# Kernel tuning notes

Hardware: AMD Instinct MI355X
Metric: run time of the kernel (lower is better)

## Reference

```python
import jax, jax.numpy as jnp
import numpy as np

B, D_K, D_V = 1024, 64, 64
N_FEAT, RANK, K = 32768, 1, 32

def _normalize(a):
    return a / jnp.linalg.norm(a, axis=-1, keepdims=True)

def setup_inputs() -> dict:
    key = jax.random.key(0)
    k0, k1, k2, k3, k4 = jax.random.split(key, 5)
    x = jax.random.normal(k0, (B, D_K, D_V), dtype=jnp.float32)
    V_enc = _normalize(jax.random.normal(k1, (N_FEAT, RANK, D_K), dtype=jnp.float32))
    W_enc = _normalize(jax.random.normal(k2, (N_FEAT, RANK, D_V), dtype=jnp.float32))
    V_dec = _normalize(jax.random.normal(k3, (N_FEAT, RANK, D_K), dtype=jnp.float32))
    W_dec = _normalize(jax.random.normal(k4, (N_FEAT, RANK, D_V), dtype=jnp.float32))
    b_enc = jnp.zeros((N_FEAT,), dtype=jnp.float32)
    bias = jnp.zeros((D_K, D_V), dtype=jnp.float32)
    return {"x": x, "V_enc": V_enc, "W_enc": W_enc, "b_enc": b_enc,
            "V_dec": V_dec, "W_dec": W_dec, "bias": bias}

def reference(x, V_enc, W_enc, b_enc, V_dec, W_dec, bias):
    b, d_k, d_v = x.shape
    n_feat = V_enc.shape[0]
    x_flat = x.reshape(b, d_k * d_v)
    # encode: einsum('irk,bkv,irv->bi') == x_flat @ (sum_r v_ir (x) w_ir)^T
    M_enc = jnp.einsum('irk,irv->ikv', V_enc, W_enc).reshape(n_feat, d_k * d_v)
    pre = x_flat @ M_enc.T + b_enc                       # [B, n_feat]
    # topk activation with relu on the kept values, zeros elsewhere
    vals, idx = jax.lax.top_k(pre, K)                    # [B, K]
    vals = jnp.maximum(vals, 0.0)
    coeffs = jnp.zeros_like(pre).at[jnp.arange(b)[:, None], idx].set(vals)
    # decode: einsum('bi,irk,irv->bkv')
    M_dec = jnp.einsum('irk,irv->ikv', V_dec, W_dec).reshape(n_feat, d_k * d_v)
    recon_flat = coeffs @ M_dec + bias.reshape(-1)
    recon = recon_flat.reshape(b, d_k, d_v)
    mse = jnp.mean((recon_flat - x_flat) ** 2)
    # fresh steps_since_active buffer (zeros) + dead_threshold=100 -> no dead
    # features, so aux_loss == 0 exactly; total loss == mse.
    return recon, coeffs, mse
```

## Files before the change

### kernel.cpp

```cpp
#include <hip/hip_runtime.h>
#include <hip/hip_bf16.h>
#include <hip/hip_fp8.h>
#include <stdint.h>

#define NFEAT 32768
#define BATCH 1024
#define DK 64
#define DV 64
#define DD 4096
#define KSEL 32
#define CAND_CAP 512
#define CAND_TARGET 128

using bf16 = __bf16;
using f32x4 = __attribute__((ext_vector_type(4))) float;
using f32x16 = __attribute__((ext_vector_type(16))) float;
using i32x4 = __attribute__((ext_vector_type(4))) int;
using i32x8 = __attribute__((ext_vector_type(8))) int;

__device__ __forceinline__ void gload_lds16(const void* g, void* l) {
  __builtin_amdgcn_global_load_lds((const __attribute__((address_space(1))) void*)g,
                                   (__attribute__((address_space(3))) void*)l,
                                   16, 0, 0);
}

__device__ inline unsigned mono16(unsigned u) {
  return (u & 0x8000u) ? ((~u) & 0xFFFFu) : (u | 0x8000u);
}


__global__ void k_convert_x(const float* __restrict__ x, unsigned char* __restrict__ xb) {
  int t = threadIdx.x;
  int rb = blockIdx.x >> 3;
  int kg0 = (blockIdx.x & 7) * 16;
  int row = (t & 127) >> 2;
  int cin = ((t >> 7) << 4) + ((t & 3) << 2);
  const float* xrow = x + ((size_t)rb * 32 + row) * DD;
  for (int kg = kg0; kg < kg0 + 16; ++kg) {
    float4 v = *reinterpret_cast<const float4*>(xrow + kg * 32 + cin);
    union { unsigned char b[4]; unsigned u; } o;
    o.b[0] = __hip_fp8_e4m3(v.x).__x;
    o.b[1] = __hip_fp8_e4m3(v.y).__x;
    o.b[2] = __hip_fp8_e4m3(v.z).__x;
    o.b[3] = __hip_fp8_e4m3(v.w).__x;
    *reinterpret_cast<unsigned*>(xb + (((size_t)rb * 128 + kg) << 10) + t * 4) = o.u;
  }
}

__global__ void k_build_menc(const float* __restrict__ Venc, const float* __restrict__ Wenc,
                             unsigned char* __restrict__ Menc) {
  int t = threadIdx.x;
  int rb = blockIdx.x;
  int row = (t & 127) >> 2;
  int cin = ((t >> 7) << 4) + ((t & 3) << 2);
  size_t rowg = (size_t)rb * 32 + row;
  const float* vrow = Venc + rowg * DK;
  float4 w0 = *reinterpret_cast<const float4*>(Wenc + rowg * DV + cin);
  float4 w1 = *reinterpret_cast<const float4*>(Wenc + rowg * DV + 32 + cin);
  unsigned char* base = Menc + ((size_t)rb << 17);
#pragma unroll 4
  for (int kg = 0; kg < 128; ++kg) {
    float vk = 16.0f * vrow[kg >> 1];
    float4 w = (kg & 1) ? w1 : w0;
    union { unsigned char b[4]; unsigned u; } o;
    o.b[0] = __hip_fp8_e4m3(vk * w.x).__x;
    o.b[1] = __hip_fp8_e4m3(vk * w.y).__x;
    o.b[2] = __hip_fp8_e4m3(vk * w.z).__x;
    o.b[3] = __hip_fp8_e4m3(vk * w.w).__x;
    *reinterpret_cast<unsigned*>(base + (kg << 10) + t * 4) = o.u;
  }
}

#define BM 256
#define BN 256
#define BKB 128
#define NT (DD / BKB)
#define ABUF 32768
#define BUFSZ 65536
#define GEMM_LDS (2 * BUFSZ)

__device__ __forceinline__ void stage_chunk(const unsigned char* __restrict__ G, size_t r32base,
                                            int kg0, int c, int lane, char* dstbase) {
  const unsigned char* src = G + (((r32base + (c >> 2)) * 128 + kg0 + (c & 3)) << 10) + lane * 16;
  gload_lds16(src, dstbase + c * 1024);
}

__device__ __forceinline__ i32x8 frag_ld8(const char* base, int chunk, int lane) {
  const char* p = base + chunk * 1024 + (lane & 31) * 16;
  i32x4 lo = *reinterpret_cast<const i32x4*>(p);
  i32x4 hi = *reinterpret_cast<const i32x4*>(p + 512);
  i32x8 r;
  r[0] = lo[0]; r[1] = lo[1]; r[2] = lo[2]; r[3] = lo[3];
  r[4] = hi[0]; r[5] = hi[1]; r[6] = hi[2]; r[7] = hi[3];
  return r;
}

__device__ __forceinline__ int chA(int half, int idx) {
  int g = idx >> 2, kg = idx & 3;
  int mb32 = (g & 1) + ((g >> 1) << 2) + half * 2;
  return mb32 * 4 + kg;
}
__device__ __forceinline__ int chB(int half, int idx) {
  int nb32 = ((idx >> 2) << 1) + half;
  return nb32 * 4 + (idx & 3);
}

#define LD_A(H)                                                                     \
  _Pragma("unroll") for (int mb = 0; mb < 2; ++mb)                                  \
  _Pragma("unroll") for (int kh = 0; kh < 2; ++kh)                                  \
    afr[mb][kh] = frag_ld8(cur, (wr * 4 + (H) * 2 + mb) * 4 + kh * 2 + (lane >> 5), lane);

#define LD_B(H)                                                                     \
  _Pragma("unroll") for (int kh = 0; kh < 2; ++kh)                                  \
    bfr[(H)][kh] = frag_ld8(cur + ABUF, (wc * 2 + (H)) * 4 + kh * 2 + (lane >> 5), lane);

#define ST_A(HALF, KT)                                                              \
  stage_chunk(A, ar32, (KT) * 4, chA(HALF, wave * 2), lane, nxt);                   \
  stage_chunk(A, ar32, (KT) * 4, chA(HALF, wave * 2 + 1), lane, nxt);

#define ST_B(HALF, KT)                                                              \
  stage_chunk(Bt, br32, (KT) * 4, chB(HALF, wave * 2), lane, nxt + ABUF);           \
  stage_chunk(Bt, br32, (KT) * 4, chB(HALF, wave * 2 + 1), lane, nxt + ABUF);

#define MFMA_Q(MH, NB)                                                              \
  asm volatile("s_waitcnt lgkmcnt(0)" ::: "memory");                                \
  __builtin_amdgcn_sched_barrier(0);                                                \
  __builtin_amdgcn_s_setprio(1);                                                    \
  _Pragma("unroll") for (int mb = 0; mb < 2; ++mb)                                  \
  _Pragma("unroll") for (int kh = 0; kh < 2; ++kh)                                  \
    acc[(MH) * 2 + mb][NB] = __builtin_amdgcn_mfma_scale_f32_32x32x64_f8f6f4(       \
        afr[mb][kh], bfr[NB][kh], acc[(MH) * 2 + mb][NB], 0, 0, 0, 0x7F, 0, 0x7F);  \
  __builtin_amdgcn_s_setprio(0);

#define VMC(N) asm volatile("s_waitcnt vmcnt(" #N ")" ::: "memory");
#define LGKM0 asm volatile("s_waitcnt lgkmcnt(0)" ::: "memory");
#define BARR                                                                        \
  asm volatile("s_barrier" ::: "memory");                                           \
  __builtin_amdgcn_sched_barrier(0);

__global__ __launch_bounds__(512, 2)
void k_gemm(const unsigned char* __restrict__ A, const unsigned char* __restrict__ Bt,
            const float* __restrict__ benc, bf16* __restrict__ C) {
  extern __shared__ char lds[];
  int tid = threadIdx.x;
  int wave = tid >> 6;
  int lane = tid & 63;
  int wr = wave >> 2;
  int wc = wave & 3;

  int d = blockIdx.x;
  int lw = (d & 7) * 64 + (d >> 3);
  int q = lw >> 2;
  int p = lw & 3;
  size_t brow = (size_t)p * BM;
  size_t bcol = (size_t)q * BN;
  size_t ar32 = brow >> 5;
  size_t br32 = bcol >> 5;

  f32x16 acc[4][2] = {};
  i32x8 afr[2][2];
  i32x8 bfr[2][2];

  {
    char* nxt = lds;
    ST_B(0, 0) ST_A(0, 0) ST_B(1, 0) ST_A(1, 0)
  }
  VMC(4)
  BARR

#pragma unroll 1
  for (int u = 0; u < NT - 1; ++u) {
    char* cur = lds + (u & 1) * BUFSZ;
    char* nxt = lds + ((u + 1) & 1) * BUFSZ;
    int k1 = u + 1;
    LD_A(0) LD_B(0)
    ST_B(0, k1)
    VMC(4)
    BARR
    MFMA_Q(0, 0)
    LD_B(1)
    ST_A(0, k1)
    VMC(4)
    BARR
    MFMA_Q(0, 1)
    LD_A(1)
    ST_B(1, k1) ST_A(1, k1)
    VMC(4)
    LGKM0
    BARR
    MFMA_Q(1, 1)
    MFMA_Q(1, 0)
  }

  {
    char* cur = lds + ((NT - 1) & 1) * BUFSZ;
    LD_A(0) LD_B(0)
    VMC(2)
    BARR
    MFMA_Q(0, 0)
    LD_B(1)
    VMC(0)
    BARR
    MFMA_Q(0, 1)
    LD_A(1)
    LGKM0
    BARR
    MFMA_Q(1, 1)
    MFMA_Q(1, 0)
  }

#pragma unroll
  for (int nb = 0; nb < 2; ++nb) {
    size_t col = bcol + wc * 64 + nb * 32 + (lane & 31);
    float be = benc[col];
#pragma unroll
    for (int MB = 0; MB < 4; ++MB) {
      size_t row0 = brow + wr * 128 + MB * 32 + ((lane >> 5) << 2);
#pragma unroll
      for (int reg = 0; reg < 16; ++reg) {
        size_t row = row0 + (reg & 3) + ((reg >> 2) << 3);
        C[row * NFEAT + col] = (bf16)(acc[MB][nb][reg] * 0.0625f + be);
      }
    }
  }
}

__global__ void k_topk(const unsigned short* __restrict__ pre, int* __restrict__ cand_idx,
                       int* __restrict__ cand_cnt, float* __restrict__ coeffs) {
  __shared__ int hist[8192];
  __shared__ int csum[256];
  __shared__ int sBstar;
  __shared__ int scount;
  int b = blockIdx.x;
  int t = threadIdx.x;
  const unsigned short* row = pre + (size_t)b * NFEAT;
  for (int i = t; i < 8192; i += 256) hist[i] = 0;
  if (t == 0) scount = 0;
  __syncthreads();

  for (int i = (t << 3); i < NFEAT; i += 2048) {
    uint4 v = *reinterpret_cast<const uint4*>(row + i);
#pragma unroll
    for (int j = 0; j < 4; ++j) {
      unsigned w = (&v.x)[j];
      atomicAdd(&hist[mono16(w & 0xFFFFu) >> 3], 1);
      atomicAdd(&hist[mono16(w >> 16) >> 3], 1);
    }
  }
  __syncthreads();

  int s = 0;
  for (int i = 0; i < 32; ++i) s += hist[t * 32 + i];
  csum[t] = s;
  __syncthreads();
  int suff = 0;
  for (int j = t + 1; j < 256; ++j) suff += csum[j];
  if (suff < CAND_TARGET && suff + s >= CAND_TARGET) {
    int acc = suff;
    int bstar = t * 32;
    for (int i = 31; i >= 0; --i) {
      acc += hist[t * 32 + i];
      if (acc >= CAND_TARGET) { bstar = t * 32 + i; break; }
    }
    sBstar = bstar;
  }
  __syncthreads();
  int Bstar = sBstar;
  int* cidx = cand_idx + b * CAND_CAP;

  for (int i = (t << 3); i < NFEAT; i += 2048) {
    uint4 v = *reinterpret_cast<const uint4*>(row + i);
#pragma unroll
    for (int j = 0; j < 4; ++j) {
      unsigned w = (&v.x)[j];
      int b0 = (int)(mono16(w & 0xFFFFu) >> 3);
      int b1 = (int)(mono16(w >> 16) >> 3);
      if (b0 >= Bstar) { int p2 = atomicAdd(&scount, 1); if (p2 < CAND_CAP) cidx[p2] = i + j * 2; }
      if (b1 >= Bstar) { int p2 = atomicAdd(&scount, 1); if (p2 < CAND_CAP) cidx[p2] = i + j * 2 + 1; }
    }
  }
  __syncthreads();
  if (t == 0) cand_cnt[b] = (scount < CAND_CAP) ? scount : CAND_CAP;

  float* crow = coeffs + (size_t)b * NFEAT;
  float4 z4 = {0.f, 0.f, 0.f, 0.f};
  for (int i = (t << 2); i < NFEAT; i += 1024)
    *reinterpret_cast<float4*>(crow + i) = z4;
}

__global__ void k_refine(const float* __restrict__ x,
                         const float* __restrict__ Venc,
                         const float* __restrict__ Wenc,
                         const float* __restrict__ benc,
                         const float* __restrict__ Vdec,
                         const float* __restrict__ Wdec,
                         const float* __restrict__ bias,
                         const int* __restrict__ cand_idx,
                         const int* __restrict__ cand_cnt,
                         float* __restrict__ recon,
                         float* __restrict__ coeffs,
                         float* __restrict__ msepart) {
  __shared__ float rval[CAND_CAP];
  __shared__ int ridx[CAND_CAP];
  __shared__ float selv[KSEL];
  __shared__ int seli[KSEL];
  __shared__ float Vd[KSEL][DK];
  __shared__ float Wd[KSEL][DV];
  __shared__ float red[256];

  int b = blockIdx.x;
  int t = threadIdx.x;
  int wave = t >> 6;
  int lane = t & 63;

  const float* xr = x + (size_t)b * DD;

  float xreg[DK];
#pragma unroll
  for (int kk = 0; kk < DK; ++kk)
    xreg[kk] = xr[kk * DV + lane];

  int c = cand_cnt[b];
  if (c > CAND_CAP) c = CAND_CAP;
  for (int i = t; i < c; i += 256) ridx[i] = cand_idx[b * CAND_CAP + i];
  __syncthreads();

  for (int j = wave; j < c; j += 4) {
    int fi = __builtin_amdgcn_readfirstlane(ridx[j]);
    const float* vr = Venc + (size_t)fi * DK;
    float w = Wenc[(size_t)fi * DV + lane];
    float a0 = 0.f, a1 = 0.f, a2 = 0.f, a3 = 0.f;
#pragma unroll
    for (int kk = 0; kk < DK; kk += 4) {
      a0 = fmaf(xreg[kk + 0], vr[kk + 0], a0);
      a1 = fmaf(xreg[kk + 1], vr[kk + 1], a1);
      a2 = fmaf(xreg[kk + 2], vr[kk + 2], a2);
      a3 = fmaf(xreg[kk + 3], vr[kk + 3], a3);
    }
    float p2 = ((a0 + a1) + (a2 + a3)) * w;
#pragma unroll
    for (int off = 1; off < 64; off <<= 1) p2 += __shfl_xor(p2, off);
    if (lane == 0) rval[j] = p2 + benc[fi];
  }
  __syncthreads();

  for (int t2 = t; t2 < c; t2 += 256) {
    float v = rval[t2];
    int fi = ridx[t2];
    int rank = 0;
    for (int j = 0; j < c; ++j) {
      float vj = rval[j];
      if (vj > v || (vj == v && ridx[j] < fi)) ++rank;
    }
    if (rank < KSEL) { selv[rank] = v; seli[rank] = fi; }
  }
  __syncthreads();

  if (t < KSEL) {
    float v = fmaxf(selv[t], 0.f);
    selv[t] = v;
    coeffs[(size_t)b * NFEAT + seli[t]] = v;
  }
  __syncthreads();

  for (int i = t; i < KSEL * DK; i += 256) {
    int s = i >> 6, e = i & 63;
    Vd[s][e] = Vdec[(size_t)seli[s] * DK + e];
    Wd[s][e] = Wdec[(size_t)seli[s] * DV + e];
  }
  __syncthreads();

  int k = t >> 2;
  int vb = (t & 3) << 4;
  float4 r4[4];
#pragma unroll
  for (int g = 0; g < 4; ++g)
    r4[g] = *reinterpret_cast<const float4*>(bias + k * DV + vb + g * 4);
#pragma unroll
  for (int s = 0; s < KSEL; ++s) {
    float a = selv[s] * Vd[s][k];
    const float4* wrow = reinterpret_cast<const float4*>(&Wd[s][vb]);
#pragma unroll
    for (int g = 0; g < 4; ++g) {
      float4 wv = wrow[g];
      r4[g].x = fmaf(a, wv.x, r4[g].x);
      r4[g].y = fmaf(a, wv.y, r4[g].y);
      r4[g].z = fmaf(a, wv.z, r4[g].z);
      r4[g].w = fmaf(a, wv.w, r4[g].w);
    }
  }
  float m = 0.f;
  float* ro = recon + (size_t)b * DD + k * DV + vb;
#pragma unroll
  for (int g = 0; g < 4; ++g) {
    float4 xv = *reinterpret_cast<const float4*>(xr + k * DV + vb + g * 4);
    float dx = r4[g].x - xv.x, dy = r4[g].y - xv.y;
    float dz = r4[g].z - xv.z, dw = r4[g].w - xv.w;
    m = fmaf(dx, dx, m); m = fmaf(dy, dy, m);
    m = fmaf(dz, dz, m); m = fmaf(dw, dw, m);
    *reinterpret_cast<float4*>(ro + g * 4) = r4[g];
  }
  red[t] = m;
  __syncthreads();
  for (int s2 = 128; s2 > 0; s2 >>= 1) {
    if (t < s2) red[t] += red[t + s2];
    __syncthreads();
  }
  if (t == 0) msepart[b] = red[0];
}

__global__ void k_mse(const float* __restrict__ msepart, float* __restrict__ out) {
  __shared__ float red[256];
  int t = threadIdx.x;
  float s = 0.f;
  for (int i = t; i < BATCH; i += 256) s += msepart[i];
  red[t] = s;
  __syncthreads();
  for (int k = 128; k > 0; k >>= 1) {
    if (t < k) red[t] += red[t + k];
    __syncthreads();
  }
  if (t == 0) out[0] = red[0] / (float)((size_t)BATCH * DD);
}

extern "C" void kernel_launch(void* const* d_in, const int* in_sizes, int n_in,
                              void* d_out, int out_size, void* d_ws, size_t ws_size,
                              hipStream_t stream) {
  const float* x    = (const float*)d_in[0];
  const float* Venc = (const float*)d_in[1];
  const float* Wenc = (const float*)d_in[2];
  const float* benc = (const float*)d_in[3];
  const float* Vdec = (const float*)d_in[4];
  const float* Wdec = (const float*)d_in[5];
  const float* bias = (const float*)d_in[6];

  float* out = (float*)d_out;
  float* recon  = out;
  float* coeffs = out + (size_t)BATCH * DD;
  float* mse    = coeffs + (size_t)BATCH * NFEAT;

  char* wsp = (char*)d_ws;
  unsigned char* xb8 = (unsigned char*)wsp;   wsp += (size_t)BATCH * DD;
  unsigned char* Menc8 = (unsigned char*)wsp; wsp += (size_t)NFEAT * DD;
  int* cand_idx = (int*)wsp;                  wsp += (size_t)BATCH * CAND_CAP * sizeof(int);
  int* cand_cnt = (int*)wsp;                  wsp += (size_t)BATCH * sizeof(int);
  float* msepart = (float*)wsp;               wsp += (size_t)BATCH * sizeof(float);
  bf16* pre = (bf16*)wsp;                     wsp += (size_t)BATCH * NFEAT * sizeof(bf16);

  hipFuncSetAttribute((const void*)k_gemm, hipFuncAttributeMaxDynamicSharedMemorySize,
                      GEMM_LDS);

  k_convert_x<<<256, 256, 0, stream>>>(x, xb8);
  k_build_menc<<<NFEAT / 32, 256, 0, stream>>>(Venc, Wenc, Menc8);
  k_gemm<<<(BATCH / BM) * (NFEAT / BN), 512, GEMM_LDS, stream>>>(xb8, Menc8, benc, pre);
  k_topk<<<BATCH, 256, 0, stream>>>((const unsigned short*)pre, cand_idx, cand_cnt, coeffs);
  k_refine<<<BATCH, 256, 0, stream>>>(x, Venc, Wenc, benc, Vdec, Wdec, bias,
                                      cand_idx, cand_cnt, recon, coeffs, msepart);
  k_mse<<<1, 256, 0, stream>>>(msepart, mse);
}
```

Before: 296.3 us.

## Fuse top-k candidate selection with refine/decode and cut GEMM barriers

Merges the histogram top-k candidate kernel and the refine/decode kernel into a single per-row kernel. Candidates stay in LDS instead of going through global memory, the coeff zeroing is folded into the histogram pass, and the Vd/Wd tiles reuse the histogram buffer. The GEMM main loop is also restructured to issue more loads per stage with fewer barriers. The fused kernel uses more LDS and registers per block, which may lower occupancy. Removing barriers and waitcnts in the GEMM tail risks LDS hazards.

```diff
diff --git a/kernel.cpp b/kernel.cpp
--- a/kernel.cpp
+++ b/kernel.cpp
@@ -165,7 +165,7 @@
     char* nxt = lds;
     ST_B(0, 0) ST_A(0, 0) ST_B(1, 0) ST_A(1, 0)
   }
-  VMC(4)
+  VMC(2)
   BARR
 
 #pragma unroll 1
@@ -173,19 +173,15 @@
     char* cur = lds + (u & 1) * BUFSZ;
     char* nxt = lds + ((u + 1) & 1) * BUFSZ;
     int k1 = u + 1;
-    LD_A(0) LD_B(0)
-    ST_B(0, k1)
-    VMC(4)
+    LD_A(0) LD_B(0) LD_B(1)
+    ST_B(0, k1) ST_A(0, k1) ST_B(1, k1)
+    VMC(6)
     BARR
     MFMA_Q(0, 0)
-    LD_B(1)
-    ST_A(0, k1)
-    VMC(4)
-    BARR
     MFMA_Q(0, 1)
     LD_A(1)
-    ST_B(1, k1) ST_A(1, k1)
-    VMC(4)
+    ST_A(1, k1)
+    VMC(2)
     LGKM0
     BARR
     MFMA_Q(1, 1)
@@ -194,17 +190,12 @@
 
   {
     char* cur = lds + ((NT - 1) & 1) * BUFSZ;
-    LD_A(0) LD_B(0)
-    VMC(2)
+    LD_A(0) LD_B(0) LD_B(1)
+    VMC(0)
     BARR
     MFMA_Q(0, 0)
-    LD_B(1)
-    VMC(0)
-    BARR
     MFMA_Q(0, 1)
     LD_A(1)
-    LGKM0
-    BARR
     MFMA_Q(1, 1)
     MFMA_Q(1, 0)
   }
@@ -225,19 +216,48 @@
   }
 }
 
-__global__ void k_topk(const unsigned short* __restrict__ pre, int* __restrict__ cand_idx,
-                       int* __restrict__ cand_cnt, float* __restrict__ coeffs) {
-  __shared__ int hist[8192];
+__global__ void k_select(const unsigned short* __restrict__ pre,
+                         const float* __restrict__ x,
+                         const float* __restrict__ Venc,
+                         const float* __restrict__ Wenc,
+                         const float* __restrict__ benc,
+                         const float* __restrict__ Vdec,
+                         const float* __restrict__ Wdec,
+                         const float* __restrict__ bias,
+                         float* __restrict__ recon,
+                         float* __restrict__ coeffs,
+                         float* __restrict__ msepart) {
+  __shared__ __align__(16) int hist[8192];
   __shared__ int csum[256];
   __shared__ int sBstar;
   __shared__ int scount;
+  __shared__ float rval[CAND_CAP];
+  __shared__ int ridx[CAND_CAP];
+  __shared__ float selv[KSEL];
+  __shared__ int seli[KSEL];
+  __shared__ float red[256];
+  float (*Vd)[DK] = (float(*)[DK])hist;
+  float (*Wd)[DV] = (float(*)[DV])(hist + 2048);
+
   int b = blockIdx.x;
   int t = threadIdx.x;
+  int wave = t >> 6;
+  int lane = t & 63;
+
   const unsigned short* row = pre + (size_t)b * NFEAT;
+  const float* xr = x + (size_t)b * DD;
+  float* crow = coeffs + (size_t)b * NFEAT;
+
+  float xreg[DK];
+#pragma unroll
+  for (int kk = 0; kk < DK; ++kk)
+    xreg[kk] = xr[kk * DV + lane];
+
   for (int i = t; i < 8192; i += 256) hist[i] = 0;
   if (t == 0) scount = 0;
   __syncthreads();
 
+  float4 z4 = {0.f, 0.f, 0.f, 0.f};
   for (int i = (t << 3); i < NFEAT; i += 2048) {
     uint4 v = *reinterpret_cast<const uint4*>(row + i);
 #pragma unroll
@@ -246,6 +266,8 @@
       atomicAdd(&hist[mono16(w & 0xFFFFu) >> 3], 1);
       atomicAdd(&hist[mono16(w >> 16) >> 3], 1);
     }
+    *reinterpret_cast<float4*>(crow + i) = z4;
+    *reinterpret_cast<float4*>(crow + i + 4) = z4;
   }
   __syncthreads();
 
@@ -266,7 +288,6 @@
   }
   __syncthreads();
   int Bstar = sBstar;
-  int* cidx = cand_idx + b * CAND_CAP;
 
   for (int i = (t << 3); i < NFEAT; i += 2048) {
     uint4 v = *reinterpret_cast<const uint4*>(row + i);
@@ -275,55 +296,13 @@
       unsigned w = (&v.x)[j];
       int b0 = (int)(mono16(w & 0xFFFFu) >> 3);
       int b1 = (int)(mono16(w >> 16) >> 3);
-      if (b0 >= Bstar) { int p2 = atomicAdd(&scount, 1); if (p2 < CAND_CAP) cidx[p2] = i + j * 2; }
-      if (b1 >= Bstar) { int p2 = atomicAdd(&scount, 1); if (p2 < CAND_CAP) cidx[p2] = i + j * 2 + 1; }
-    }
-  }
-  __syncthreads();
-  if (t == 0) cand_cnt[b] = (scount < CAND_CAP) ? scount : CAND_CAP;
-
-  float* crow = coeffs + (size_t)b * NFEAT;
-  float4 z4 = {0.f, 0.f, 0.f, 0.f};
-  for (int i = (t << 2); i < NFEAT; i += 1024)
-    *reinterpret_cast<float4*>(crow + i) = z4;
-}
-
-__global__ void k_refine(const float* __restrict__ x,
-                         const float* __restrict__ Venc,
-                         const float* __restrict__ Wenc,
-                         const float* __restrict__ benc,
-                         const float* __restrict__ Vdec,
-                         const float* __restrict__ Wdec,
-                         const float* __restrict__ bias,
-                         const int* __restrict__ cand_idx,
-                         const int* __restrict__ cand_cnt,
-                         float* __restrict__ recon,
-                         float* __restrict__ coeffs,
-                         float* __restrict__ msepart) {
-  __shared__ float rval[CAND_CAP];
-  __shared__ int ridx[CAND_CAP];
-  __shared__ float selv[KSEL];
-  __shared__ int seli[KSEL];
-  __shared__ float Vd[KSEL][DK];
-  __shared__ float Wd[KSEL][DV];
-  __shared__ float red[256];
-
-  int b = blockIdx.x;
-  int t = threadIdx.x;
-  int wave = t >> 6;
-  int lane = t & 63;
-
-  const float* xr = x + (size_t)b * DD;
-
-  float xreg[DK];
-#pragma unroll
-  for (int kk = 0; kk < DK; ++kk)
-    xreg[kk] = xr[kk * DV + lane];
-
-  int c = cand_cnt[b];
+      if (b0 >= Bstar) { int p2 = atomicAdd(&scount, 1); if (p2 < CAND_CAP) ridx[p2] = i + j * 2; }
+      if (b1 >= Bstar) { int p2 = atomicAdd(&scount, 1); if (p2 < CAND_CAP) ridx[p2] = i + j * 2 + 1; }
+    }
+  }
+  __syncthreads();
+  int c = scount;
   if (c > CAND_CAP) c = CAND_CAP;
-  for (int i = t; i < c; i += 256) ridx[i] = cand_idx[b * CAND_CAP + i];
-  __syncthreads();
 
   for (int j = wave; j < c; j += 4) {
     int fi = __builtin_amdgcn_readfirstlane(ridx[j]);
@@ -359,14 +338,14 @@
   if (t < KSEL) {
     float v = fmaxf(selv[t], 0.f);
     selv[t] = v;
-    coeffs[(size_t)b * NFEAT + seli[t]] = v;
+    crow[seli[t]] = v;
   }
   __syncthreads();
 
   for (int i = t; i < KSEL * DK; i += 256) {
-    int s = i >> 6, e = i & 63;
-    Vd[s][e] = Vdec[(size_t)seli[s] * DK + e];
-    Wd[s][e] = Wdec[(size_t)seli[s] * DV + e];
+    int s2 = i >> 6, e = i & 63;
+    Vd[s2][e] = Vdec[(size_t)seli[s2] * DK + e];
+    Wd[s2][e] = Wdec[(size_t)seli[s2] * DV + e];
   }
   __syncthreads();
 
@@ -377,9 +356,9 @@
   for (int g = 0; g < 4; ++g)
     r4[g] = *reinterpret_cast<const float4*>(bias + k * DV + vb + g * 4);
 #pragma unroll
-  for (int s = 0; s < KSEL; ++s) {
-    float a = selv[s] * Vd[s][k];
-    const float4* wrow = reinterpret_cast<const float4*>(&Wd[s][vb]);
+  for (int s2 = 0; s2 < KSEL; ++s2) {
+    float a = selv[s2] * Vd[s2][k];
+    const float4* wrow = reinterpret_cast<const float4*>(&Wd[s2][vb]);
 #pragma unroll
     for (int g = 0; g < 4; ++g) {
       float4 wv = wrow[g];
@@ -442,8 +421,6 @@
   char* wsp = (char*)d_ws;
   unsigned char* xb8 = (unsigned char*)wsp;   wsp += (size_t)BATCH * DD;
   unsigned char* Menc8 = (unsigned char*)wsp; wsp += (size_t)NFEAT * DD;
-  int* cand_idx = (int*)wsp;                  wsp += (size_t)BATCH * CAND_CAP * sizeof(int);
-  int* cand_cnt = (int*)wsp;                  wsp += (size_t)BATCH * sizeof(int);
   float* msepart = (float*)wsp;               wsp += (size_t)BATCH * sizeof(float);
   bf16* pre = (bf16*)wsp;                     wsp += (size_t)BATCH * NFEAT * sizeof(bf16);
 
@@ -453,8 +430,7 @@
   k_convert_x<<<256, 256, 0, stream>>>(x, xb8);
   k_build_menc<<<NFEAT / 32, 256, 0, stream>>>(Venc, Wenc, Menc8);
   k_gemm<<<(BATCH / BM) * (NFEAT / BN), 512, GEMM_LDS, stream>>>(xb8, Menc8, benc, pre);
-  k_topk<<<BATCH, 256, 0, stream>>>((const unsigned short*)pre, cand_idx, cand_cnt, coeffs);
-  k_refine<<<BATCH, 256, 0, stream>>>(x, Venc, Wenc, benc, Vdec, Wdec, bias,
-                                      cand_idx, cand_cnt, recon, coeffs, msepart);
+  k_select<<<BATCH, 256, 0, stream>>>((const unsigned short*)pre, x, Venc, Wenc, benc,
+                                      Vdec, Wdec, bias, recon, coeffs, msepart);
   k_mse<<<1, 256, 0, stream>>>(msepart, mse);
 }
```

Measured after the change: 304.5 us. 2.8% more time.
